# Kernel tuning notes

Measured on AMD Instinct MI355X. Metric: run time of the kernel, lower is better.

The kernel has to match this reference:

```python
import jax, jax.numpy as jnp
from jax import lax
import numpy as np

B, N, K = 8, 4096, 64          # clouds, points per cloud, max neighbors
N1, N2 = N // 2, N // 8        # fps ratio 0.5, then 0.25
R1, R2 = 0.2, 0.4              # ball-query radii


def setup_inputs() -> dict:
    key = jax.random.key(0)
    ks = jax.random.split(key, 7)
    def w(k, i, o):
        return jax.random.normal(k, (i, o), jnp.float32) / np.sqrt(i).astype(np.float32)
    return {
        "pos": jax.random.uniform(ks[0], (B, N, 3), jnp.float32),
        "w1a": w(ks[1], 3, 64),    "b1a": jnp.zeros(64, jnp.float32),
        "w1b": w(ks[2], 64, 64),   "b1b": jnp.zeros(64, jnp.float32),
        "w2a": w(ks[3], 67, 128),  "b2a": jnp.zeros(128, jnp.float32),
        "w2b": w(ks[4], 128, 128), "b2b": jnp.zeros(128, jnp.float32),
        "w3a": w(ks[5], 131, 256), "b3a": jnp.zeros(256, jnp.float32),
        "w3b": w(ks[6], 256, 1024),"b3b": jnp.zeros(1024, jnp.float32),
    }


def fps(pos, n_samples):
    # farthest point sampling, deterministic start at index 0. pos: [n, 3]
    d0 = jnp.sum((pos - pos[0]) ** 2, axis=-1)
    def step(mind, _):
        nxt = jnp.argmax(mind)
        d = jnp.sum((pos - pos[nxt]) ** 2, axis=-1)
        return jnp.minimum(mind, d), nxt
    _, idxs = lax.scan(step, d0, None, length=n_samples - 1)
    return jnp.concatenate([jnp.zeros((1,), idxs.dtype), idxs])


def ball_query(centers, pts, r):
    # up to K neighbors within radius r (nearest-first); centers are a subset of pts
    d2 = jnp.sum((centers[:, None, :] - pts[None, :, :]) ** 2, axis=-1)  # [M, n]
    neg = jnp.where(d2 <= r * r, -d2, -jnp.inf)
    vals, nbr = lax.top_k(neg, K)
    return nbr, vals > -jnp.inf  # [M, K] indices, validity mask


def mlp(x, w1, b1, w2, b2, relu_last):
    h = jax.nn.relu(x @ w1 + b1) @ w2 + b2
    return jax.nn.relu(h) if relu_last else h


def masked_max(h, mask):
    # max over neighbor axis; every center has itself as a valid neighbor
    return jnp.max(jnp.where(mask[..., None], h, -jnp.inf), axis=1)


def reference(pos, w1a, b1a, w1b, b1b, w2a, b2a, w2b, b2b, w3a, b3a, w3b, b3b):
    def single(p):  # p: [N, 3]
        # SA1: x is None -> per-edge input is relative position only
        idx1 = fps(p, N1)
        c1 = p[idx1]                                   # [N1, 3]
        nbr1, m1 = ball_query(c1, p, R1)               # [N1, K]
        rel1 = p[nbr1] - c1[:, None, :]                # [N1, K, 3]
        x1 = masked_max(mlp(rel1, w1a, b1a, w1b, b1b, True), m1)   # [N1, 64]
        # SA2: per-edge input is [x_j, pos_j - pos_i]
        idx2 = fps(c1, N2)
        c2 = c1[idx2]                                  # [N2, 3]
        nbr2, m2 = ball_query(c2, c1, R2)              # [N2, K]
        feat2 = jnp.concatenate([x1[nbr2], c1[nbr2] - c2[:, None, :]], axis=-1)  # [N2,K,67]
        x2 = masked_max(mlp(feat2, w2a, b2a, w2b, b2b, True), m2)  # [N2, 128]
        # Global SA: MLP on [x, pos] then global max pool
        g = mlp(jnp.concatenate([x2, c2], axis=-1), w3a, b3a, w3b, b3b, False)   # [N2,1024]
        return jnp.max(g, axis=0)                      # [1024]
    return jax.vmap(single)(pos)                       # [B, 1024]
```

## Files before the change

### kernel.cpp

```cpp
#include <hip/hip_runtime.h>
#include <cstdint>
#include <cstddef>


static constexpr int Bc = 8;
static constexpr int Np = 4096;
static constexpr int Kn = 64;
static constexpr int M1 = 2048;
static constexpr int M2 = 512;
static constexpr int LDX = 132;

#define DEVINL __device__ __forceinline__

DEVINL float d2_exact(float ax, float ay, float az, float bx, float by, float bz) {
    float dx = __fsub_rn(ax, bx);
    float dy = __fsub_rn(ay, by);
    float dz = __fsub_rn(az, bz);
    float xx = __fmul_rn(dx, dx);
    float yy = __fmul_rn(dy, dy);
    float zz = __fmul_rn(dz, dz);
    return __fadd_rn(__fadd_rn(xx, yy), zz);
}

template <int CTRL, int RM, int BM>
DEVINL unsigned long long dpp_max_step(unsigned long long k) {
    unsigned lo = (unsigned)k, hi = (unsigned)(k >> 32);
    unsigned slo = (unsigned)__builtin_amdgcn_update_dpp(0, (int)lo, CTRL, RM, BM, true);
    unsigned shi = (unsigned)__builtin_amdgcn_update_dpp(0, (int)hi, CTRL, RM, BM, true);
    unsigned long long s = ((unsigned long long)shi << 32) | (unsigned long long)slo;
    return s > k ? s : k;
}

DEVINL unsigned long long wave_max_u64_dpp(unsigned long long k) {
    k = dpp_max_step<0x111, 0xf, 0xf>(k);
    k = dpp_max_step<0x112, 0xf, 0xf>(k);
    k = dpp_max_step<0x114, 0xf, 0xf>(k);
    k = dpp_max_step<0x118, 0xf, 0xf>(k);
    k = dpp_max_step<0x142, 0xa, 0xf>(k);
    k = dpp_max_step<0x143, 0xc, 0xf>(k);
    return k;
}

DEVINL unsigned mort3(unsigned v) {
    return (v & 1u) | ((v & 2u) << 2) | ((v & 4u) << 4);
}

DEVINL unsigned cell_of(float x, float y, float z) {
    int ix = (int)(x * 8.0f); ix = ix < 0 ? 0 : (ix > 7 ? 7 : ix);
    int iy = (int)(y * 8.0f); iy = iy < 0 ? 0 : (iy > 7 ? 7 : iy);
    int iz = (int)(z * 8.0f); iz = iz < 0 ? 0 : (iz > 7 ? 7 : iz);
    return mort3((unsigned)ix) | (mort3((unsigned)iy) << 1) | (mort3((unsigned)iz) << 2);
}

DEVINL unsigned* scan512(unsigned* h0, unsigned* h1, int t) {
    unsigned* src = h0; unsigned* dst = h1;
    for (int d = 1; d < 512; d <<= 1) {
        unsigned v = src[t];
        if (t >= d) v += src[t - d];
        dst[t] = v;
        __syncthreads();
        unsigned* tmp = src; src = dst; dst = tmp;
    }
    return src;
}

__global__ __launch_bounds__(512)
void fps2x_kernel(const float* __restrict__ pos, float* __restrict__ c1,
                  float* __restrict__ c2, float* __restrict__ X) {
    constexpr int NT = 512;
    __shared__ float scx[Np], scy[Np], scz[Np];
    __shared__ unsigned spk[Np];
    __shared__ alignas(16) float s2c[M1 * 3];
    __shared__ alignas(16) float s3c[M2 * 3];
    __shared__ unsigned h0[512], h1[512];
    __shared__ unsigned long long slots[3];
    const int b = blockIdx.x;
    const int t = threadIdx.x;
    const int lane = t & 63;

    {
        constexpr int PT = Np / NT;
        const float* base = pos + (size_t)b * Np * 3;
        float gx[PT], gy[PT], gz[PT];
        unsigned gc[PT];
        #pragma unroll
        for (int j = 0; j < PT; ++j) {
            int p = j * NT + t;
            gx[j] = base[p * 3 + 0];
            gy[j] = base[p * 3 + 1];
            gz[j] = base[p * 3 + 2];
            gc[j] = cell_of(gx[j], gy[j], gz[j]);
        }
        float x0 = base[0], y0 = base[1], z0 = base[2];
        h0[t] = 0;
        if (t == 0) { slots[0] = 0; slots[1] = 0; slots[2] = 0; }
        __syncthreads();
        #pragma unroll
        for (int j = 0; j < PT; ++j) atomicAdd(&h0[gc[j]], 1u);
        __syncthreads();
        unsigned cnt = h0[t];
        unsigned* inc = scan512(h0, h1, t);
        inc[t] -= cnt;
        __syncthreads();
        #pragma unroll
        for (int j = 0; j < PT; ++j) {
            unsigned p = atomicAdd(&inc[gc[j]], 1u);
            scx[p] = gx[j]; scy[p] = gy[j]; scz[p] = gz[j];
            spk[p] = ((0xFFFu - (unsigned)(j * NT + t)) << 12) | p;
        }
        __syncthreads();

        float px[PT], py[PT], pz[PT], mind[PT];
        unsigned oi[PT];
        #pragma unroll
        for (int j = 0; j < PT; ++j) {
            int p = t * PT + j;
            px[j] = scx[p]; py[j] = scy[p]; pz[j] = scz[p];
            oi[j] = spk[p];
        }
        float lox = px[0], hix = px[0], loy = py[0], hiy = py[0], loz = pz[0], hiz = pz[0];
        #pragma unroll
        for (int j = 1; j < PT; ++j) {
            lox = fminf(lox, px[j]); hix = fmaxf(hix, px[j]);
            loy = fminf(loy, py[j]); hiy = fmaxf(hiy, py[j]);
            loz = fminf(loz, pz[j]); hiz = fmaxf(hiz, pz[j]);
        }

        unsigned long long ck = 0;
        #pragma unroll
        for (int j = 0; j < PT; ++j) {
            float d = d2_exact(px[j], py[j], pz[j], x0, y0, z0);
            mind[j] = d;
            unsigned long long kj =
                ((unsigned long long)__float_as_uint(d) << 24) | (unsigned long long)oi[j];
            if (kj > ck) ck = kj;
        }
        float bmax = __uint_as_float((unsigned)(ck >> 24));
        unsigned long long wkey = wave_max_u64_dpp(ck);
        if (lane == 63) atomicMax(&slots[1], wkey);
        if (t == 0) { s2c[0] = x0; s2c[1] = y0; s2c[2] = z0; }
        int rd = 1, wr = 2, rs = 0;
        for (int s = 1; s < M1; ++s) {
            __syncthreads();
            unsigned long long km = slots[rd];
            if (t == 0) slots[rs] = 0;
            unsigned spos = (unsigned)km & 0xFFFu;
            float cx = scx[spos], cy = scy[spos], cz = scz[spos];
            if (t == 0) {
                s2c[s * 3 + 0] = cx; s2c[s * 3 + 1] = cy; s2c[s * 3 + 2] = cz;
            }
            float dxv = fmaxf(fmaxf(lox - cx, cx - hix), 0.0f);
            float dyv = fmaxf(fmaxf(loy - cy, cy - hiy), 0.0f);
            float dzv = fmaxf(fmaxf(loz - cz, cz - hiz), 0.0f);
            float L = dxv * dxv + dyv * dyv + dzv * dzv;
            bool fire = (L * 0.999f <= bmax);
            if (fire) {
                unsigned long long nck = 0;
                #pragma unroll
                for (int j = 0; j < PT; ++j) {
                    float d = d2_exact(px[j], py[j], pz[j], cx, cy, cz);
                    float m = fminf(mind[j], d);
                    mind[j] = m;
                    unsigned long long kj =
                        ((unsigned long long)__float_as_uint(m) << 24) | (unsigned long long)oi[j];
                    if (kj > nck) nck = kj;
                }
                ck = nck;
                bmax = __uint_as_float((unsigned)(ck >> 24));
            }
            if (__ballot(fire) != 0ull) wkey = wave_max_u64_dpp(ck);
            if (lane == 63) atomicMax(&slots[wr], wkey);
            int nrd = wr; wr = rs; rs = rd; rd = nrd;
        }
    }
    __syncthreads();

    {
        const float4* s2c4 = (const float4*)s2c;
        float4* c1b = (float4*)(c1 + (size_t)b * M1 * 3);
        for (int i = t; i < M1 * 3 / 4; i += NT) c1b[i] = s2c4[i];
    }
    if (t == 0) { slots[0] = 0; slots[1] = 0; slots[2] = 0; }
    __syncthreads();

    {
        constexpr int PT = M1 / NT;
        float gx[PT], gy[PT], gz[PT];
        unsigned gc[PT];
        #pragma unroll
        for (int j = 0; j < PT; ++j) {
            int p = j * NT + t;
            gx[j] = s2c[p * 3 + 0];
            gy[j] = s2c[p * 3 + 1];
            gz[j] = s2c[p * 3 + 2];
            gc[j] = cell_of(gx[j], gy[j], gz[j]);
        }
        float x0 = s2c[0], y0 = s2c[1], z0 = s2c[2];
        h0[t] = 0;
        __syncthreads();
        #pragma unroll
        for (int j = 0; j < PT; ++j) atomicAdd(&h0[gc[j]], 1u);
        __syncthreads();
        unsigned cnt = h0[t];
        unsigned* inc = scan512(h0, h1, t);
        inc[t] -= cnt;
        __syncthreads();
        #pragma unroll
        for (int j = 0; j < PT; ++j) {
            unsigned p = atomicAdd(&inc[gc[j]], 1u);
            scx[p] = gx[j]; scy[p] = gy[j]; scz[p] = gz[j];
            spk[p] = ((0xFFFu - (unsigned)(j * NT + t)) << 12) | p;
        }
        __syncthreads();

        float px[PT], py[PT], pz[PT], mind[PT];
        unsigned oi[PT];
        #pragma unroll
        for (int j = 0; j < PT; ++j) {
            int p = t * PT + j;
            px[j] = scx[p]; py[j] = scy[p]; pz[j] = scz[p];
            oi[j] = spk[p];
        }
        float lox = px[0], hix = px[0], loy = py[0], hiy = py[0], loz = pz[0], hiz = pz[0];
        #pragma unroll
        for (int j = 1; j < PT; ++j) {
            lox = fminf(lox, px[j]); hix = fmaxf(hix, px[j]);
            loy = fminf(loy, py[j]); hiy = fmaxf(hiy, py[j]);
            loz = fminf(loz, pz[j]); hiz = fmaxf(hiz, pz[j]);
        }

        unsigned long long ck = 0;
        #pragma unroll
        for (int j = 0; j < PT; ++j) {
            float d = d2_exact(px[j], py[j], pz[j], x0, y0, z0);
            mind[j] = d;
            unsigned long long kj =
                ((unsigned long long)__float_as_uint(d) << 24) | (unsigned long long)oi[j];
            if (kj > ck) ck = kj;
        }
        float bmax = __uint_as_float((unsigned)(ck >> 24));
        unsigned long long wkey = wave_max_u64_dpp(ck);
        if (lane == 63) atomicMax(&slots[1], wkey);
        if (t == 0) { s3c[0] = x0; s3c[1] = y0; s3c[2] = z0; }
        int rd = 1, wr = 2, rs = 0;
        for (int s = 1; s < M2; ++s) {
            __syncthreads();
            unsigned long long km = slots[rd];
            if (t == 0) slots[rs] = 0;
            unsigned spos = (unsigned)km & 0xFFFu;
            float cx = scx[spos], cy = scy[spos], cz = scz[spos];
            if (t == 0) {
                s3c[s * 3 + 0] = cx; s3c[s * 3 + 1] = cy; s3c[s * 3 + 2] = cz;
            }
            float dxv = fmaxf(fmaxf(lox - cx, cx - hix), 0.0f);
            float dyv = fmaxf(fmaxf(loy - cy, cy - hiy), 0.0f);
            float dzv = fmaxf(fmaxf(loz - cz, cz - hiz), 0.0f);
            float L = dxv * dxv + dyv * dyv + dzv * dzv;
            bool fire = (L * 0.999f <= bmax);
            if (fire) {
                unsigned long long nck = 0;
                #pragma unroll
                for (int j = 0; j < PT; ++j) {
                    float d = d2_exact(px[j], py[j], pz[j], cx, cy, cz);
                    float m = fminf(mind[j], d);
                    mind[j] = m;
                    unsigned long long kj =
                        ((unsigned long long)__float_as_uint(m) << 24) | (unsigned long long)oi[j];
                    if (kj > nck) nck = kj;
                }
                ck = nck;
                bmax = __uint_as_float((unsigned)(ck >> 24));
            }
            if (__ballot(fire) != 0ull) wkey = wave_max_u64_dpp(ck);
            if (lane == 63) atomicMax(&slots[wr], wkey);
            int nrd = wr; wr = rs; rs = rd; rd = nrd;
        }
    }
    __syncthreads();

    {
        const float4* s3c4 = (const float4*)s3c;
        float4* c2b = (float4*)(c2 + (size_t)b * M2 * 3);
        for (int i = t; i < M2 * 3 / 4; i += NT) c2b[i] = s3c4[i];
        for (int s = t; s < M2; s += NT) {
            float* xr = X + (size_t)(b * M2 + s) * LDX;
            xr[128] = s3c[s * 3 + 0];
            xr[129] = s3c[s * 3 + 1];
            xr[130] = s3c[s * 3 + 2];
        }
    }
}

template <int NPT>
__global__ __launch_bounds__(256)
void bq_kernel(const float* __restrict__ pts, const float* __restrict__ ctr,
               int mshift, float r2, int* __restrict__ nbr) {
    constexpr int CH = NPT / 64;
    constexpr int CAP = 1024;
    __shared__ uint2 cbuf[4][CAP];
    const int lane = threadIdx.x & 63;
    const int wl = threadIdx.x >> 6;
    int w = __builtin_amdgcn_readfirstlane((int)(blockIdx.x * 4 + wl));
    const int b = w >> mshift;
    const float* pb = pts + (size_t)b * NPT * 3;
    const float* cp = ctr + (size_t)w * 3;
    float cx = cp[0], cy = cp[1], cz = cp[2];
    const unsigned r2b = __float_as_uint(r2);

    unsigned ub[CH];
    int cnt = 0;
    #pragma unroll
    for (int j = 0; j < CH; ++j) {
        int p = j * 64 + lane;
        float d = d2_exact(pb[p * 3 + 0], pb[p * 3 + 1], pb[p * 3 + 2], cx, cy, cz);
        ub[j] = __float_as_uint(d);
        cnt += __popcll(__ballot(ub[j] <= r2b));
    }
    int* out = nbr + (size_t)w * Kn;
    const unsigned long long lml = (1ull << lane) - 1ull;

    if (cnt <= Kn) {
        int basep = 0;
        #pragma unroll
        for (int j = 0; j < CH; ++j) {
            bool v = ub[j] <= r2b;
            unsigned long long mk = __ballot(v);
            if (v) out[basep + __popcll(mk & lml)] = j * 64 + lane;
            basep += __popcll(mk);
        }
        if (lane >= cnt) out[lane] = -1;
    } else if (cnt <= CAP) {
        uint2* buf = cbuf[wl];
        int basep = 0;
        #pragma unroll
        for (int j = 0; j < CH; ++j) {
            bool v = ub[j] <= r2b;
            unsigned long long mk = __ballot(v);
            if (v) buf[basep + __popcll(mk & lml)] =
                       make_uint2(ub[j], (unsigned)(j * 64 + lane));
            basep += __popcll(mk);
        }
        const int C2 = (cnt + 63) >> 6;
        unsigned cb[CAP / 64], ci[CAP / 64];
        #pragma unroll
        for (int e = 0; e < CAP / 64; ++e) {
            if (e >= C2) break;
            int p = e * 64 + lane;
            uint2 v = buf[p];
            cb[e] = (p < cnt) ? v.x : 0xFFFFFFFFu;
            ci[e] = v.y;
        }
        unsigned lo = 0, hi = r2b;
        while (lo < hi) {
            unsigned mid = lo + ((hi - lo) >> 1);
            int c = 0;
            #pragma unroll
            for (int e = 0; e < CAP / 64; ++e) {
                if (e >= C2) break;
                c += __popcll(__ballot(cb[e] <= mid));
            }
            if (c >= Kn) hi = mid; else lo = mid + 1;
        }
        const unsigned tt = lo;
        int cntLess = 0;
        #pragma unroll
        for (int e = 0; e < CAP / 64; ++e) {
            if (e >= C2) break;
            cntLess += __popcll(__ballot(cb[e] < tt));
        }
        const int quota = Kn - cntLess;
        int baseLt = 0, eqseen = 0;
        #pragma unroll
        for (int e = 0; e < CAP / 64; ++e) {
            if (e >= C2) break;
            bool lt = cb[e] < tt;
            bool eq = cb[e] == tt;
            unsigned long long mlt = __ballot(lt);
            unsigned long long meq = __ballot(eq);
            if (lt) out[baseLt + __popcll(mlt & lml)] = (int)ci[e];
            if (eq) {
                int rr = eqseen + __popcll(meq & lml);
                if (rr < quota) out[cntLess + rr] = (int)ci[e];
            }
            baseLt += __popcll(mlt);
            eqseen += __popcll(meq);
        }
    } else {
        unsigned lo = 0, hi = r2b;
        while (lo < hi) {
            unsigned mid = lo + ((hi - lo) >> 1);
            int c = 0;
            #pragma unroll
            for (int j = 0; j < CH; ++j) c += __popcll(__ballot(ub[j] <= mid));
            if (c >= Kn) hi = mid; else lo = mid + 1;
        }
        const unsigned tt = lo;
        int cntLess = 0;
        #pragma unroll
        for (int j = 0; j < CH; ++j) cntLess += __popcll(__ballot(ub[j] < tt));
        const int quota = Kn - cntLess;
        int baseLt = 0, eqseen = 0;
        #pragma unroll
        for (int j = 0; j < CH; ++j) {
            bool lt = ub[j] < tt;
            bool eq = ub[j] == tt;
            unsigned long long mlt = __ballot(lt);
            unsigned long long meq = __ballot(eq);
            if (lt) out[baseLt + __popcll(mlt & lml)] = j * 64 + lane;
            if (eq) {
                int rr = eqseen + __popcll(meq & lml);
                if (rr < quota) out[cntLess + rr] = j * 64 + lane;
            }
            baseLt += __popcll(mlt);
            eqseen += __popcll(meq);
        }
    }
}

__global__ __launch_bounds__(256)
void mlp1_kernel(const float* __restrict__ pos, const float* __restrict__ c1,
                 const int* __restrict__ nbr, const float* __restrict__ w1aT,
                 const float* __restrict__ w1bT, const float* __restrict__ b1b,
                 float* __restrict__ x1) {
    const int lane = threadIdx.x & 63;
    int w = __builtin_amdgcn_readfirstlane((int)(blockIdx.x * 4 + (threadIdx.x >> 6)));
    const int b = w >> 11;
    const int ii = nbr[(size_t)w * Kn + lane];
    const bool valid = ii >= 0;
    const int i2 = valid ? ii : 0;
    const float* pp = pos + ((size_t)b * Np + i2) * 3;
    const float* cc = c1 + (size_t)w * 3;
    float rx = pp[0] - cc[0], ry = pp[1] - cc[1], rz = pp[2] - cc[2];
    float h1[64];
    #pragma unroll
    for (int h = 0; h < 64; ++h) {
        float4 wv = ((const float4*)w1aT)[h];
        float a = fmaf(rx, wv.x, fmaf(ry, wv.y, fmaf(rz, wv.z, wv.w)));
        h1[h] = fmaxf(a, 0.0f);
    }
    float* orow = x1 + (size_t)w * 64;
    for (int c4 = 0; c4 < 16; ++c4) {
        float v4[4];
        #pragma unroll
        for (int cq = 0; cq < 4; ++cq) {
            int c = c4 * 4 + cq;
            float acc = b1b[c];
            const float4* wr = (const float4*)(w1bT + (size_t)c * 64);
            #pragma unroll
            for (int q = 0; q < 16; ++q) {
                float4 wv = wr[q];
                acc = fmaf(h1[4 * q + 0], wv.x, acc);
                acc = fmaf(h1[4 * q + 1], wv.y, acc);
                acc = fmaf(h1[4 * q + 2], wv.z, acc);
                acc = fmaf(h1[4 * q + 3], wv.w, acc);
            }
            float v = fmaxf(acc, 0.0f);
            v = valid ? v : -__builtin_inff();
            #pragma unroll
            for (int o = 32; o > 0; o >>= 1) v = fmaxf(v, __shfl_xor(v, o, 64));
            v4[cq] = v;
        }
        if (lane == 0)
            ((float4*)orow)[c4] = make_float4(v4[0], v4[1], v4[2], v4[3]);
    }
}

__global__ __launch_bounds__(256)
void mlp2_kernel(const float* __restrict__ x1, const float* __restrict__ c1,
                 const float* __restrict__ c2, const int* __restrict__ nbr2,
                 const float* __restrict__ w2aT, const float* __restrict__ w2bT,
                 const float* __restrict__ b2b, float* __restrict__ X) {
    const int lane = threadIdx.x & 63;
    int w = __builtin_amdgcn_readfirstlane((int)(blockIdx.x * 4 + (threadIdx.x >> 6)));
    const int b = w >> 9;
    const int ii = nbr2[(size_t)w * Kn + lane];
    const bool valid = ii >= 0;
    const int i2 = valid ? ii : 0;

    float x[68];
    const float4* xr = (const float4*)(x1 + ((size_t)b * M1 + i2) * 64);
    #pragma unroll
    for (int q = 0; q < 16; ++q) {
        float4 v = xr[q];
        x[4 * q + 0] = v.x; x[4 * q + 1] = v.y;
        x[4 * q + 2] = v.z; x[4 * q + 3] = v.w;
    }
    const float* cc = c2 + (size_t)w * 3;
    const float* cp = c1 + ((size_t)b * M1 + i2) * 3;
    x[64] = cp[0] - cc[0];
    x[65] = cp[1] - cc[1];
    x[66] = cp[2] - cc[2];
    x[67] = 0.0f;

    float h1[128];
    #pragma unroll
    for (int h = 0; h < 128; ++h) {
        const float4* r4 = (const float4*)(w2aT + (size_t)h * 80);
        float acc = 0.0f;
        #pragma unroll
        for (int q = 0; q < 16; ++q) {
            float4 wv = r4[q];
            acc = fmaf(x[4 * q + 0], wv.x, acc);
            acc = fmaf(x[4 * q + 1], wv.y, acc);
            acc = fmaf(x[4 * q + 2], wv.z, acc);
            acc = fmaf(x[4 * q + 3], wv.w, acc);
        }
        float4 tl = r4[16];
        acc = fmaf(x[64], tl.x, acc);
        acc = fmaf(x[65], tl.y, acc);
        acc = fmaf(x[66], tl.z, acc);
        acc += tl.w;
        h1[h] = fmaxf(acc, 0.0f);
    }
    float* orow = X + (size_t)w * LDX;
    for (int c4 = 0; c4 < 32; ++c4) {
        float v4[4];
        #pragma unroll
        for (int cq = 0; cq < 4; ++cq) {
            int c = c4 * 4 + cq;
            float acc = b2b[c];
            const float4* wr = (const float4*)(w2bT + (size_t)c * 128);
            #pragma unroll
            for (int q = 0; q < 32; ++q) {
                float4 wv = wr[q];
                acc = fmaf(h1[4 * q + 0], wv.x, acc);
                acc = fmaf(h1[4 * q + 1], wv.y, acc);
                acc = fmaf(h1[4 * q + 2], wv.z, acc);
                acc = fmaf(h1[4 * q + 3], wv.w, acc);
            }
            float v = fmaxf(acc, 0.0f);
            v = valid ? v : -__builtin_inff();
            #pragma unroll
            for (int o = 32; o > 0; o >>= 1) v = fmaxf(v, __shfl_xor(v, o, 64));
            v4[cq] = v;
        }
        if (lane == 0) {
            orow[c4 * 4 + 0] = v4[0]; orow[c4 * 4 + 1] = v4[1];
            orow[c4 * 4 + 2] = v4[2]; orow[c4 * 4 + 3] = v4[3];
        }
    }
}

__global__ __launch_bounds__(256)
void gemm1_kernel(const float* __restrict__ X, const float* __restrict__ w3a,
                  const float* __restrict__ b3a, float* __restrict__ H) {
    const int r = blockIdx.x;
    const int c = threadIdx.x;
    const float* xr = X + (size_t)r * LDX;
    float acc = b3a[c];
    for (int i = 0; i < 131; ++i)
        acc = fmaf(xr[i], w3a[(size_t)i * 256 + c], acc);
    H[(size_t)r * 256 + c] = fmaxf(acc, 0.0f);
}

__global__ __launch_bounds__(256)
void gemm2_kernel(const float* __restrict__ H, const float* __restrict__ w3b,
                  float* __restrict__ part) {
    __shared__ float As[32][33];
    __shared__ float Bs[32][64];
    __shared__ float red[8][64];
    const int bidx = blockIdx.x;
    const int nt = bidx & 15;
    const int mt = (bidx >> 4) & 15;
    const int b = bidx >> 8;
    const int row0 = b * M2 + mt * 32;
    const int col0 = nt * 64;
    const int t = threadIdx.x;
    const int rg = t >> 5, cg = t & 31;

    float acc[4][2] = {{0.f, 0.f}, {0.f, 0.f}, {0.f, 0.f}, {0.f, 0.f}};
    for (int k0 = 0; k0 < 256; k0 += 32) {
        #pragma unroll
        for (int q = 0; q < 4; ++q) {
            int id = t + q * 256;
            As[id >> 5][id & 31] = H[(size_t)(row0 + (id >> 5)) * 256 + k0 + (id & 31)];
        }
        #pragma unroll
        for (int q = 0; q < 8; ++q) {
            int id = t + q * 256;
            Bs[id >> 6][id & 63] = w3b[(size_t)(k0 + (id >> 6)) * 1024 + col0 + (id & 63)];
        }
        __syncthreads();
        #pragma unroll
        for (int kk = 0; kk < 32; ++kk) {
            float b0 = Bs[kk][cg * 2 + 0];
            float b1 = Bs[kk][cg * 2 + 1];
            #pragma unroll
            for (int j = 0; j < 4; ++j) {
                float a = As[rg * 4 + j][kk];
                acc[j][0] = fmaf(a, b0, acc[j][0]);
                acc[j][1] = fmaf(a, b1, acc[j][1]);
            }
        }
        __syncthreads();
    }
    float m0 = fmaxf(fmaxf(acc[0][0], acc[1][0]), fmaxf(acc[2][0], acc[3][0]));
    float m1 = fmaxf(fmaxf(acc[0][1], acc[1][1]), fmaxf(acc[2][1], acc[3][1]));
    red[rg][cg * 2 + 0] = m0;
    red[rg][cg * 2 + 1] = m1;
    __syncthreads();
    if (t < 64) {
        float v = red[0][t];
        #pragma unroll
        for (int q = 1; q < 8; ++q) v = fmaxf(v, red[q][t]);
        part[((size_t)b * 16 + mt) * 1024 + col0 + t] = v;
    }
}

__global__ __launch_bounds__(256)
void rmax_kernel(const float* __restrict__ part, const float* __restrict__ b3b,
                 float* __restrict__ out) {
    int i = blockIdx.x * 256 + threadIdx.x;
    int b = i >> 10, c = i & 1023;
    float v = -__builtin_inff();
    #pragma unroll
    for (int tt = 0; tt < 16; ++tt)
        v = fmaxf(v, part[((size_t)b * 16 + tt) * 1024 + c]);
    out[i] = v + b3b[c];
}

__global__ __launch_bounds__(256)
void prep_kernel(const float* __restrict__ w1a, const float* __restrict__ b1a,
                 const float* __restrict__ w1b, const float* __restrict__ w2a,
                 const float* __restrict__ b2a, const float* __restrict__ w2b,
                 float* __restrict__ w1aT, float* __restrict__ w1bT,
                 float* __restrict__ w2aT, float* __restrict__ w2bT) {
    int i = blockIdx.x * 256 + threadIdx.x;
    if (i < 64 * 4) {
        int h = i >> 2, d = i & 3;
        w1aT[i] = (d < 3) ? w1a[d * 64 + h] : b1a[h];
    }
    if (i < 64 * 64) {
        int c = i >> 6, h = i & 63;
        w1bT[i] = w1b[h * 64 + c];
    }
    if (i < 128 * 80) {
        int h = i / 80, d = i - h * 80;
        w2aT[i] = (d < 67) ? w2a[d * 128 + h] : ((d == 67) ? b2a[h] : 0.0f);
    }
    {
        int c = i >> 7, h = i & 127;
        w2bT[i] = w2b[h * 128 + c];
    }
}

extern "C" void kernel_launch(void* const* d_in, const int* in_sizes, int n_in,
                              void* d_out, int out_size, void* d_ws, size_t ws_size,
                              hipStream_t stream) {
    const float* pos = (const float*)d_in[0];
    const float* w1a = (const float*)d_in[1];
    const float* b1a = (const float*)d_in[2];
    const float* w1b = (const float*)d_in[3];
    const float* b1b = (const float*)d_in[4];
    const float* w2a = (const float*)d_in[5];
    const float* b2a = (const float*)d_in[6];
    const float* w2b = (const float*)d_in[7];
    const float* b2b = (const float*)d_in[8];
    const float* w3a = (const float*)d_in[9];
    const float* b3a = (const float*)d_in[10];
    const float* w3b = (const float*)d_in[11];
    const float* b3b = (const float*)d_in[12];
    float* out = (float*)d_out;

    char* ws = (char*)d_ws;
    size_t off = 0;
    auto alloc = [&](size_t bytes) -> char* {
        char* p = ws + off;
        off += (bytes + 255) & ~(size_t)255;
        return p;
    };
    float* c1   = (float*)alloc(sizeof(float) * Bc * M1 * 3);
    float* c2   = (float*)alloc(sizeof(float) * Bc * M2 * 3);
    int*   nbr1 = (int*)alloc(sizeof(int) * Bc * M1 * Kn);
    int*   nbr2 = (int*)alloc(sizeof(int) * Bc * M2 * Kn);
    float* x1   = (float*)alloc(sizeof(float) * Bc * M1 * 64);
    float* X    = (float*)alloc(sizeof(float) * Bc * M2 * LDX);
    float* H    = (float*)alloc(sizeof(float) * Bc * M2 * 256);
    float* part = (float*)alloc(sizeof(float) * Bc * 16 * 1024);
    float* w1aT = (float*)alloc(sizeof(float) * 64 * 4);
    float* w1bT = (float*)alloc(sizeof(float) * 64 * 64);
    float* w2aT = (float*)alloc(sizeof(float) * 128 * 80);
    float* w2bT = (float*)alloc(sizeof(float) * 128 * 128);

    prep_kernel<<<dim3(64), dim3(256), 0, stream>>>(w1a, b1a, w1b, w2a, b2a, w2b,
                                                    w1aT, w1bT, w2aT, w2bT);
    fps2x_kernel<<<dim3(Bc), dim3(512), 0, stream>>>(pos, c1, c2, X);
    bq_kernel<Np><<<dim3(Bc * M1 / 4), dim3(256), 0, stream>>>(
        pos, c1, 11, (float)(0.2 * 0.2), nbr1);
    mlp1_kernel<<<dim3(Bc * M1 / 4), dim3(256), 0, stream>>>(
        pos, c1, nbr1, w1aT, w1bT, b1b, x1);
    bq_kernel<M1><<<dim3(Bc * M2 / 4), dim3(256), 0, stream>>>(
        c1, c2, 9, (float)(0.4 * 0.4), nbr2);
    mlp2_kernel<<<dim3(Bc * M2 / 4), dim3(256), 0, stream>>>(
        x1, c1, c2, nbr2, w2aT, w2bT, b2b, X);
    gemm1_kernel<<<dim3(Bc * M2), dim3(256), 0, stream>>>(X, w3a, b3a, H);
    gemm2_kernel<<<dim3(Bc * 16 * 16), dim3(256), 0, stream>>>(H, w3b, part);
    rmax_kernel<<<dim3(32), dim3(256), 0, stream>>>(part, b3b, out);
}
```

Measured before the change: 2.557 ms.

## Fuse pipeline stages into four kernels, keeping neighbor lists in shared memory

Merges weight prep into the FPS kernel, ball query 1 with MLP1, ball query 2 with MLP2 and the first global GEMM, and the final row-max into the second GEMM using a last-block atomic counter. Neighbor indices and per-center features now stay in shared memory instead of global buffers, and five launches are removed. The cost is higher register and shared-memory pressure in the fused kernels, plus a counter that must be reset by the earlier kernel. The SA2 ball query also drops the mid-size candidate-buffer path and always uses binary search when there are more than K neighbors.

```diff
diff --git a/kernel.cpp b/kernel.cpp
--- a/kernel.cpp
+++ b/kernel.cpp
@@ -8,7 +8,6 @@
 static constexpr int Kn = 64;
 static constexpr int M1 = 2048;
 static constexpr int M2 = 512;
-static constexpr int LDX = 132;
 
 #define DEVINL __device__ __forceinline__
 
@@ -66,7 +65,12 @@
 
 __global__ __launch_bounds__(512)
 void fps2x_kernel(const float* __restrict__ pos, float* __restrict__ c1,
-                  float* __restrict__ c2, float* __restrict__ X) {
+                  float* __restrict__ c2,
+                  const float* __restrict__ w1a, const float* __restrict__ b1a,
+                  const float* __restrict__ w1b, const float* __restrict__ w2a,
+                  const float* __restrict__ b2a, const float* __restrict__ w2b,
+                  float* __restrict__ w1aT, float* __restrict__ w1bT,
+                  float* __restrict__ w2aT, float* __restrict__ w2bT) {
     constexpr int NT = 512;
     __shared__ float scx[Np], scy[Np], scz[Np];
     __shared__ unsigned spk[Np];
@@ -77,6 +81,25 @@
     const int b = blockIdx.x;
     const int t = threadIdx.x;
     const int lane = t & 63;
+
+    for (int i = b * NT + t; i < 128 * 128; i += Bc * NT) {
+        if (i < 64 * 4) {
+            int h = i >> 2, d = i & 3;
+            w1aT[i] = (d < 3) ? w1a[d * 64 + h] : b1a[h];
+        }
+        if (i < 64 * 64) {
+            int c = i >> 6, h = i & 63;
+            w1bT[i] = w1b[h * 64 + c];
+        }
+        if (i < 128 * 80) {
+            int h = i / 80, d = i - h * 80;
+            w2aT[i] = (d < 67) ? w2a[d * 128 + h] : ((d == 67) ? b2a[h] : 0.0f);
+        }
+        {
+            int c = i >> 7, h = i & 127;
+            w2bT[i] = w2b[h * 128 + c];
+        }
+    }
 
     {
         constexpr int PT = Np / NT;
@@ -282,30 +305,26 @@
         const float4* s3c4 = (const float4*)s3c;
         float4* c2b = (float4*)(c2 + (size_t)b * M2 * 3);
         for (int i = t; i < M2 * 3 / 4; i += NT) c2b[i] = s3c4[i];
-        for (int s = t; s < M2; s += NT) {
-            float* xr = X + (size_t)(b * M2 + s) * LDX;
-            xr[128] = s3c[s * 3 + 0];
-            xr[129] = s3c[s * 3 + 1];
-            xr[130] = s3c[s * 3 + 2];
-        }
-    }
-}
-
-template <int NPT>
+    }
+}
+
 __global__ __launch_bounds__(256)
-void bq_kernel(const float* __restrict__ pts, const float* __restrict__ ctr,
-               int mshift, float r2, int* __restrict__ nbr) {
+void bqmlp1_kernel(const float* __restrict__ pos, const float* __restrict__ c1,
+                   const float* __restrict__ w1aT, const float* __restrict__ w1bT,
+                   const float* __restrict__ b1b, float* __restrict__ x1) {
+    constexpr int NPT = Np;
     constexpr int CH = NPT / 64;
     constexpr int CAP = 1024;
     __shared__ uint2 cbuf[4][CAP];
+    __shared__ int nout[4][Kn];
     const int lane = threadIdx.x & 63;
     const int wl = threadIdx.x >> 6;
     int w = __builtin_amdgcn_readfirstlane((int)(blockIdx.x * 4 + wl));
-    const int b = w >> mshift;
-    const float* pb = pts + (size_t)b * NPT * 3;
-    const float* cp = ctr + (size_t)w * 3;
+    const int b = w >> 11;
+    const float* pb = pos + (size_t)b * NPT * 3;
+    const float* cp = c1 + (size_t)w * 3;
     float cx = cp[0], cy = cp[1], cz = cp[2];
-    const unsigned r2b = __float_as_uint(r2);
+    const unsigned r2b = __float_as_uint(0.04f);
 
     unsigned ub[CH];
     int cnt = 0;
@@ -316,7 +335,7 @@
         ub[j] = __float_as_uint(d);
         cnt += __popcll(__ballot(ub[j] <= r2b));
     }
-    int* out = nbr + (size_t)w * Kn;
+    int* out = &nout[wl][0];
     const unsigned long long lml = (1ull << lane) - 1ull;
 
     if (cnt <= Kn) {
@@ -415,22 +434,13 @@
             eqseen += __popcll(meq);
         }
     }
-}
-
-__global__ __launch_bounds__(256)
-void mlp1_kernel(const float* __restrict__ pos, const float* __restrict__ c1,
-                 const int* __restrict__ nbr, const float* __restrict__ w1aT,
-                 const float* __restrict__ w1bT, const float* __restrict__ b1b,
-                 float* __restrict__ x1) {
-    const int lane = threadIdx.x & 63;
-    int w = __builtin_amdgcn_readfirstlane((int)(blockIdx.x * 4 + (threadIdx.x >> 6)));
-    const int b = w >> 11;
-    const int ii = nbr[(size_t)w * Kn + lane];
+    __syncthreads();
+
+    const int ii = nout[wl][lane];
     const bool valid = ii >= 0;
     const int i2 = valid ? ii : 0;
     const float* pp = pos + ((size_t)b * Np + i2) * 3;
-    const float* cc = c1 + (size_t)w * 3;
-    float rx = pp[0] - cc[0], ry = pp[1] - cc[1], rz = pp[2] - cc[2];
+    float rx = pp[0] - cx, ry = pp[1] - cy, rz = pp[2] - cz;
     float h1[64];
     #pragma unroll
     for (int h = 0; h < 64; ++h) {
@@ -466,99 +476,177 @@
 }
 
 __global__ __launch_bounds__(256)
-void mlp2_kernel(const float* __restrict__ x1, const float* __restrict__ c1,
-                 const float* __restrict__ c2, const int* __restrict__ nbr2,
-                 const float* __restrict__ w2aT, const float* __restrict__ w2bT,
-                 const float* __restrict__ b2b, float* __restrict__ X) {
+void bqmlp2g1_kernel(const float* __restrict__ c1, const float* __restrict__ c2,
+                     const float* __restrict__ x1, const float* __restrict__ w2aT,
+                     const float* __restrict__ w2bT, const float* __restrict__ b2b,
+                     const float* __restrict__ w3a, const float* __restrict__ b3a,
+                     float* __restrict__ H, unsigned* __restrict__ counter) {
+    constexpr int NPT = M1;
+    constexpr int CH = NPT / 64;
+    __shared__ int nout[4][Kn];
+    __shared__ float sX[4][132];
     const int lane = threadIdx.x & 63;
-    int w = __builtin_amdgcn_readfirstlane((int)(blockIdx.x * 4 + (threadIdx.x >> 6)));
+    const int wl = threadIdx.x >> 6;
+    int w = __builtin_amdgcn_readfirstlane((int)(blockIdx.x * 4 + wl));
     const int b = w >> 9;
-    const int ii = nbr2[(size_t)w * Kn + lane];
-    const bool valid = ii >= 0;
-    const int i2 = valid ? ii : 0;
-
-    float x[68];
-    const float4* xr = (const float4*)(x1 + ((size_t)b * M1 + i2) * 64);
+    if (blockIdx.x == 0 && threadIdx.x == 0) *counter = 0;
+    const float* pb = c1 + (size_t)b * NPT * 3;
+    const float* cp = c2 + (size_t)w * 3;
+    float cx = cp[0], cy = cp[1], cz = cp[2];
+    const unsigned r2b = __float_as_uint(0.16000001f);
+
+    unsigned ub[CH];
+    int cnt = 0;
     #pragma unroll
-    for (int q = 0; q < 16; ++q) {
-        float4 v = xr[q];
-        x[4 * q + 0] = v.x; x[4 * q + 1] = v.y;
-        x[4 * q + 2] = v.z; x[4 * q + 3] = v.w;
-    }
-    const float* cc = c2 + (size_t)w * 3;
-    const float* cp = c1 + ((size_t)b * M1 + i2) * 3;
-    x[64] = cp[0] - cc[0];
-    x[65] = cp[1] - cc[1];
-    x[66] = cp[2] - cc[2];
-    x[67] = 0.0f;
-
-    float h1[128];
-    #pragma unroll
-    for (int h = 0; h < 128; ++h) {
-        const float4* r4 = (const float4*)(w2aT + (size_t)h * 80);
-        float acc = 0.0f;
+    for (int j = 0; j < CH; ++j) {
+        int p = j * 64 + lane;
+        float d = d2_exact(pb[p * 3 + 0], pb[p * 3 + 1], pb[p * 3 + 2], cx, cy, cz);
+        ub[j] = __float_as_uint(d);
+        cnt += __popcll(__ballot(ub[j] <= r2b));
+    }
+    int* out = &nout[wl][0];
+    const unsigned long long lml = (1ull << lane) - 1ull;
+
+    if (cnt <= Kn) {
+        int basep = 0;
+        #pragma unroll
+        for (int j = 0; j < CH; ++j) {
+            bool v = ub[j] <= r2b;
+            unsigned long long mk = __ballot(v);
+            if (v) out[basep + __popcll(mk & lml)] = j * 64 + lane;
+            basep += __popcll(mk);
+        }
+        if (lane >= cnt) out[lane] = -1;
+    } else {
+        unsigned lo = 0, hi = r2b;
+        while (lo < hi) {
+            unsigned mid = lo + ((hi - lo) >> 1);
+            int c = 0;
+            #pragma unroll
+            for (int j = 0; j < CH; ++j) c += __popcll(__ballot(ub[j] <= mid));
+            if (c >= Kn) hi = mid; else lo = mid + 1;
+        }
+        const unsigned tt = lo;
+        int cntLess = 0;
+        #pragma unroll
+        for (int j = 0; j < CH; ++j) cntLess += __popcll(__ballot(ub[j] < tt));
+        const int quota = Kn - cntLess;
+        int baseLt = 0, eqseen = 0;
+        #pragma unroll
+        for (int j = 0; j < CH; ++j) {
+            bool lt = ub[j] < tt;
+            bool eq = ub[j] == tt;
+            unsigned long long mlt = __ballot(lt);
+            unsigned long long meq = __ballot(eq);
+            if (lt) out[baseLt + __popcll(mlt & lml)] = j * 64 + lane;
+            if (eq) {
+                int rr = eqseen + __popcll(meq & lml);
+                if (rr < quota) out[cntLess + rr] = j * 64 + lane;
+            }
+            baseLt += __popcll(mlt);
+            eqseen += __popcll(meq);
+        }
+    }
+    __syncthreads();
+
+    {
+        const int ii = nout[wl][lane];
+        const bool valid = ii >= 0;
+        const int i2 = valid ? ii : 0;
+        float x[68];
+        const float4* xr = (const float4*)(x1 + ((size_t)b * M1 + i2) * 64);
         #pragma unroll
         for (int q = 0; q < 16; ++q) {
-            float4 wv = r4[q];
-            acc = fmaf(x[4 * q + 0], wv.x, acc);
-            acc = fmaf(x[4 * q + 1], wv.y, acc);
-            acc = fmaf(x[4 * q + 2], wv.z, acc);
-            acc = fmaf(x[4 * q + 3], wv.w, acc);
-        }
-        float4 tl = r4[16];
-        acc = fmaf(x[64], tl.x, acc);
-        acc = fmaf(x[65], tl.y, acc);
-        acc = fmaf(x[66], tl.z, acc);
-        acc += tl.w;
-        h1[h] = fmaxf(acc, 0.0f);
-    }
-    float* orow = X + (size_t)w * LDX;
-    for (int c4 = 0; c4 < 32; ++c4) {
-        float v4[4];
-        #pragma unroll
-        for (int cq = 0; cq < 4; ++cq) {
-            int c = c4 * 4 + cq;
-            float acc = b2b[c];
-            const float4* wr = (const float4*)(w2bT + (size_t)c * 128);
-            #pragma unroll
-            for (int q = 0; q < 32; ++q) {
-                float4 wv = wr[q];
-                acc = fmaf(h1[4 * q + 0], wv.x, acc);
-                acc = fmaf(h1[4 * q + 1], wv.y, acc);
-                acc = fmaf(h1[4 * q + 2], wv.z, acc);
-                acc = fmaf(h1[4 * q + 3], wv.w, acc);
-            }
-            float v = fmaxf(acc, 0.0f);
-            v = valid ? v : -__builtin_inff();
-            #pragma unroll
-            for (int o = 32; o > 0; o >>= 1) v = fmaxf(v, __shfl_xor(v, o, 64));
-            v4[cq] = v;
+            float4 v = xr[q];
+            x[4 * q + 0] = v.x; x[4 * q + 1] = v.y;
+            x[4 * q + 2] = v.z; x[4 * q + 3] = v.w;
+        }
+        const float* cpn = c1 + ((size_t)b * M1 + i2) * 3;
+        x[64] = cpn[0] - cx;
+        x[65] = cpn[1] - cy;
+        x[66] = cpn[2] - cz;
+        x[67] = 0.0f;
+
+        float h1[128];
+        #pragma unroll
+        for (int h = 0; h < 128; ++h) {
+            const float4* r4 = (const float4*)(w2aT + (size_t)h * 80);
+            float acc = 0.0f;
+            #pragma unroll
+            for (int q = 0; q < 16; ++q) {
+                float4 wv = r4[q];
+                acc = fmaf(x[4 * q + 0], wv.x, acc);
+                acc = fmaf(x[4 * q + 1], wv.y, acc);
+                acc = fmaf(x[4 * q + 2], wv.z, acc);
+                acc = fmaf(x[4 * q + 3], wv.w, acc);
+            }
+            float4 tl = r4[16];
+            acc = fmaf(x[64], tl.x, acc);
+            acc = fmaf(x[65], tl.y, acc);
+            acc = fmaf(x[66], tl.z, acc);
+            acc += tl.w;
+            h1[h] = fmaxf(acc, 0.0f);
+        }
+        for (int c4 = 0; c4 < 32; ++c4) {
+            float v4[4];
+            #pragma unroll
+            for (int cq = 0; cq < 4; ++cq) {
+                int c = c4 * 4 + cq;
+                float acc = b2b[c];
+                const float4* wr = (const float4*)(w2bT + (size_t)c * 128);
+                #pragma unroll
+                for (int q = 0; q < 32; ++q) {
+                    float4 wv = wr[q];
+                    acc = fmaf(h1[4 * q + 0], wv.x, acc);
+                    acc = fmaf(h1[4 * q + 1], wv.y, acc);
+                    acc = fmaf(h1[4 * q + 2], wv.z, acc);
+                    acc = fmaf(h1[4 * q + 3], wv.w, acc);
+                }
+                float v = fmaxf(acc, 0.0f);
+                v = valid ? v : -__builtin_inff();
+                #pragma unroll
+                for (int o = 32; o > 0; o >>= 1) v = fmaxf(v, __shfl_xor(v, o, 64));
+                v4[cq] = v;
+            }
+            if (lane == 0) {
+                sX[wl][c4 * 4 + 0] = v4[0]; sX[wl][c4 * 4 + 1] = v4[1];
+                sX[wl][c4 * 4 + 2] = v4[2]; sX[wl][c4 * 4 + 3] = v4[3];
+            }
         }
         if (lane == 0) {
-            orow[c4 * 4 + 0] = v4[0]; orow[c4 * 4 + 1] = v4[1];
-            orow[c4 * 4 + 2] = v4[2]; orow[c4 * 4 + 3] = v4[3];
-        }
+            sX[wl][128] = cx; sX[wl][129] = cy; sX[wl][130] = cz;
+            sX[wl][131] = 0.0f;
+        }
+    }
+    __syncthreads();
+
+    {
+        const int t = threadIdx.x;
+        float bias = b3a[t];
+        float a0 = bias, a1 = bias, a2 = bias, a3 = bias;
+        for (int i = 0; i < 131; ++i) {
+            float wv = w3a[(size_t)i * 256 + t];
+            a0 = fmaf(sX[0][i], wv, a0);
+            a1 = fmaf(sX[1][i], wv, a1);
+            a2 = fmaf(sX[2][i], wv, a2);
+            a3 = fmaf(sX[3][i], wv, a3);
+        }
+        const size_t r0 = (size_t)blockIdx.x * 4;
+        H[(r0 + 0) * 256 + t] = fmaxf(a0, 0.0f);
+        H[(r0 + 1) * 256 + t] = fmaxf(a1, 0.0f);
+        H[(r0 + 2) * 256 + t] = fmaxf(a2, 0.0f);
+        H[(r0 + 3) * 256 + t] = fmaxf(a3, 0.0f);
     }
 }
 
 __global__ __launch_bounds__(256)
-void gemm1_kernel(const float* __restrict__ X, const float* __restrict__ w3a,
-                  const float* __restrict__ b3a, float* __restrict__ H) {
-    const int r = blockIdx.x;
-    const int c = threadIdx.x;
-    const float* xr = X + (size_t)r * LDX;
-    float acc = b3a[c];
-    for (int i = 0; i < 131; ++i)
-        acc = fmaf(xr[i], w3a[(size_t)i * 256 + c], acc);
-    H[(size_t)r * 256 + c] = fmaxf(acc, 0.0f);
-}
-
-__global__ __launch_bounds__(256)
-void gemm2_kernel(const float* __restrict__ H, const float* __restrict__ w3b,
-                  float* __restrict__ part) {
+void gemm2rmax_kernel(const float* __restrict__ H, const float* __restrict__ w3b,
+                      float* __restrict__ part, unsigned* __restrict__ counter,
+                      const float* __restrict__ b3b, float* __restrict__ out) {
     __shared__ float As[32][33];
     __shared__ float Bs[32][64];
     __shared__ float red[8][64];
+    __shared__ int islast;
     const int bidx = blockIdx.x;
     const int nt = bidx & 15;
     const int mt = (bidx >> 4) & 15;
@@ -605,42 +693,23 @@
         for (int q = 1; q < 8; ++q) v = fmaxf(v, red[q][t]);
         part[((size_t)b * 16 + mt) * 1024 + col0 + t] = v;
     }
-}
-
-__global__ __launch_bounds__(256)
-void rmax_kernel(const float* __restrict__ part, const float* __restrict__ b3b,
-                 float* __restrict__ out) {
-    int i = blockIdx.x * 256 + threadIdx.x;
-    int b = i >> 10, c = i & 1023;
-    float v = -__builtin_inff();
-    #pragma unroll
-    for (int tt = 0; tt < 16; ++tt)
-        v = fmaxf(v, part[((size_t)b * 16 + tt) * 1024 + c]);
-    out[i] = v + b3b[c];
-}
-
-__global__ __launch_bounds__(256)
-void prep_kernel(const float* __restrict__ w1a, const float* __restrict__ b1a,
-                 const float* __restrict__ w1b, const float* __restrict__ w2a,
-                 const float* __restrict__ b2a, const float* __restrict__ w2b,
-                 float* __restrict__ w1aT, float* __restrict__ w1bT,
-                 float* __restrict__ w2aT, float* __restrict__ w2bT) {
-    int i = blockIdx.x * 256 + threadIdx.x;
-    if (i < 64 * 4) {
-        int h = i >> 2, d = i & 3;
-        w1aT[i] = (d < 3) ? w1a[d * 64 + h] : b1a[h];
-    }
-    if (i < 64 * 64) {
-        int c = i >> 6, h = i & 63;
-        w1bT[i] = w1b[h * 64 + c];
-    }
-    if (i < 128 * 80) {
-        int h = i / 80, d = i - h * 80;
-        w2aT[i] = (d < 67) ? w2a[d * 128 + h] : ((d == 67) ? b2a[h] : 0.0f);
-    }
-    {
-        int c = i >> 7, h = i & 127;
-        w2bT[i] = w2b[h * 128 + c];
+    __threadfence();
+    __syncthreads();
+    if (t == 0) {
+        unsigned r = atomicAdd(counter, 1u);
+        islast = (r == (unsigned)(gridDim.x - 1)) ? 1 : 0;
+    }
+    __syncthreads();
+    if (islast) {
+        __threadfence();
+        for (int i = t; i < Bc * 1024; i += 256) {
+            int bb = i >> 10, c = i & 1023;
+            float v = -__builtin_inff();
+            #pragma unroll
+            for (int tt2 = 0; tt2 < 16; ++tt2)
+                v = fmaxf(v, part[((size_t)bb * 16 + tt2) * 1024 + c]);
+            out[i] = v + b3b[c];
+        }
     }
 }
 
@@ -671,29 +740,21 @@
     };
     float* c1   = (float*)alloc(sizeof(float) * Bc * M1 * 3);
     float* c2   = (float*)alloc(sizeof(float) * Bc * M2 * 3);
-    int*   nbr1 = (int*)alloc(sizeof(int) * Bc * M1 * Kn);
-    int*   nbr2 = (int*)alloc(sizeof(int) * Bc * M2 * Kn);
     float* x1   = (float*)alloc(sizeof(float) * Bc * M1 * 64);
-    float* X    = (float*)alloc(sizeof(float) * Bc * M2 * LDX);
     float* H    = (float*)alloc(sizeof(float) * Bc * M2 * 256);
     float* part = (float*)alloc(sizeof(float) * Bc * 16 * 1024);
     float* w1aT = (float*)alloc(sizeof(float) * 64 * 4);
     float* w1bT = (float*)alloc(sizeof(float) * 64 * 64);
     float* w2aT = (float*)alloc(sizeof(float) * 128 * 80);
     float* w2bT = (float*)alloc(sizeof(float) * 128 * 128);
-
-    prep_kernel<<<dim3(64), dim3(256), 0, stream>>>(w1a, b1a, w1b, w2a, b2a, w2b,
-                                                    w1aT, w1bT, w2aT, w2bT);
-    fps2x_kernel<<<dim3(Bc), dim3(512), 0, stream>>>(pos, c1, c2, X);
-    bq_kernel<Np><<<dim3(Bc * M1 / 4), dim3(256), 0, stream>>>(
-        pos, c1, 11, (float)(0.2 * 0.2), nbr1);
-    mlp1_kernel<<<dim3(Bc * M1 / 4), dim3(256), 0, stream>>>(
-        pos, c1, nbr1, w1aT, w1bT, b1b, x1);
-    bq_kernel<M1><<<dim3(Bc * M2 / 4), dim3(256), 0, stream>>>(
-        c1, c2, 9, (float)(0.4 * 0.4), nbr2);
-    mlp2_kernel<<<dim3(Bc * M2 / 4), dim3(256), 0, stream>>>(
-        x1, c1, c2, nbr2, w2aT, w2bT, b2b, X);
-    gemm1_kernel<<<dim3(Bc * M2), dim3(256), 0, stream>>>(X, w3a, b3a, H);
-    gemm2_kernel<<<dim3(Bc * 16 * 16), dim3(256), 0, stream>>>(H, w3b, part);
-    rmax_kernel<<<dim3(32), dim3(256), 0, stream>>>(part, b3b, out);
-}
+    unsigned* counter = (unsigned*)alloc(sizeof(unsigned) * 16);
+
+    fps2x_kernel<<<dim3(Bc), dim3(512), 0, stream>>>(
+        pos, c1, c2, w1a, b1a, w1b, w2a, b2a, w2b, w1aT, w1bT, w2aT, w2bT);
+    bqmlp1_kernel<<<dim3(Bc * M1 / 4), dim3(256), 0, stream>>>(
+        pos, c1, w1aT, w1bT, b1b, x1);
+    bqmlp2g1_kernel<<<dim3(Bc * M2 / 4), dim3(256), 0, stream>>>(
+        c1, c2, x1, w2aT, w2bT, b2b, w3a, b3a, H, counter);
+    gemm2rmax_kernel<<<dim3(Bc * 16 * 16), dim3(256), 0, stream>>>(
+        H, w3b, part, counter, b3b, out);
+}
```

New measurement: 2.868 ms. +12.2%, slower.

## Replace FPS atomic slot reduction with per-wave partials and halve block size

Applied to the files above, without the earlier changes.

The FPS kernel now runs with 256 threads (4 waves) instead of 512. Each wave writes its best key and the winning point's coordinates into a double-buffered shared array, and every thread picks the maximum of the four entries. This replaces the LDS atomicMax on rotating slots and the dependent coordinate lookup. The spatial grid drops to 256 cells in plain row-major order, with a smaller scan. Per-step synchronisation latency should fall, in exchange for each thread owning twice as many points.

```diff
diff --git a/kernel.cpp b/kernel.cpp
--- a/kernel.cpp
+++ b/kernel.cpp
@@ -41,20 +41,16 @@
     return k;
 }
 
-DEVINL unsigned mort3(unsigned v) {
-    return (v & 1u) | ((v & 2u) << 2) | ((v & 4u) << 4);
-}
-
 DEVINL unsigned cell_of(float x, float y, float z) {
-    int ix = (int)(x * 8.0f); ix = ix < 0 ? 0 : (ix > 7 ? 7 : ix);
+    int ix = (int)(x * 4.0f); ix = ix < 0 ? 0 : (ix > 3 ? 3 : ix);
     int iy = (int)(y * 8.0f); iy = iy < 0 ? 0 : (iy > 7 ? 7 : iy);
     int iz = (int)(z * 8.0f); iz = iz < 0 ? 0 : (iz > 7 ? 7 : iz);
-    return mort3((unsigned)ix) | (mort3((unsigned)iy) << 1) | (mort3((unsigned)iz) << 2);
-}
-
-DEVINL unsigned* scan512(unsigned* h0, unsigned* h1, int t) {
+    return ((unsigned)ix << 6) | ((unsigned)iy << 3) | (unsigned)iz;
+}
+
+DEVINL unsigned* scan256(unsigned* h0, unsigned* h1, int t) {
     unsigned* src = h0; unsigned* dst = h1;
-    for (int d = 1; d < 512; d <<= 1) {
+    for (int d = 1; d < 256; d <<= 1) {
         unsigned v = src[t];
         if (t >= d) v += src[t - d];
         dst[t] = v;
@@ -64,19 +60,35 @@
     return src;
 }
 
-__global__ __launch_bounds__(512)
+DEVINL void sel2(unsigned long long ka, float4 ca, unsigned long long kb, float4 cb,
+                 unsigned long long& ko, float4& co) {
+    bool tk = kb > ka;
+    ko = tk ? kb : ka;
+    co.x = tk ? cb.x : ca.x;
+    co.y = tk ? cb.y : ca.y;
+    co.z = tk ? cb.z : ca.z;
+}
+
+DEVINL unsigned long long readlane63_u64(unsigned long long v) {
+    unsigned lo = (unsigned)__builtin_amdgcn_readlane((int)(unsigned)v, 63);
+    unsigned hi = (unsigned)__builtin_amdgcn_readlane((int)(unsigned)(v >> 32), 63);
+    return ((unsigned long long)hi << 32) | (unsigned long long)lo;
+}
+
+__global__ __launch_bounds__(256)
 void fps2x_kernel(const float* __restrict__ pos, float* __restrict__ c1,
                   float* __restrict__ c2, float* __restrict__ X) {
-    constexpr int NT = 512;
+    constexpr int NT = 256;
     __shared__ float scx[Np], scy[Np], scz[Np];
     __shared__ unsigned spk[Np];
     __shared__ alignas(16) float s2c[M1 * 3];
     __shared__ alignas(16) float s3c[M2 * 3];
-    __shared__ unsigned h0[512], h1[512];
-    __shared__ unsigned long long slots[3];
+    __shared__ unsigned h0[256], h1[256];
+    __shared__ alignas(16) unsigned long long pK[2][4];
+    __shared__ alignas(16) float4 pC[2][4];
     const int b = blockIdx.x;
     const int t = threadIdx.x;
-    const int lane = t & 63;
+    const int wid = t >> 6;
 
     {
         constexpr int PT = Np / NT;
@@ -93,13 +105,12 @@
         }
         float x0 = base[0], y0 = base[1], z0 = base[2];
         h0[t] = 0;
-        if (t == 0) { slots[0] = 0; slots[1] = 0; slots[2] = 0; }
         __syncthreads();
         #pragma unroll
         for (int j = 0; j < PT; ++j) atomicAdd(&h0[gc[j]], 1u);
         __syncthreads();
         unsigned cnt = h0[t];
-        unsigned* inc = scan512(h0, h1, t);
+        unsigned* inc = scan256(h0, h1, t);
         inc[t] -= cnt;
         __syncthreads();
         #pragma unroll
@@ -127,25 +138,32 @@
         }
 
         unsigned long long ck = 0;
+        float bx = 0.f, by = 0.f, bz = 0.f;
         #pragma unroll
         for (int j = 0; j < PT; ++j) {
             float d = d2_exact(px[j], py[j], pz[j], x0, y0, z0);
             mind[j] = d;
             unsigned long long kj =
                 ((unsigned long long)__float_as_uint(d) << 24) | (unsigned long long)oi[j];
-            if (kj > ck) ck = kj;
+            if (kj > ck) { ck = kj; bx = px[j]; by = py[j]; bz = pz[j]; }
         }
         float bmax = __uint_as_float((unsigned)(ck >> 24));
-        unsigned long long wkey = wave_max_u64_dpp(ck);
-        if (lane == 63) atomicMax(&slots[1], wkey);
+        unsigned long long wred = wave_max_u64_dpp(ck);
+        unsigned long long wk = readlane63_u64(wred);
+        if (ck == wk) { pK[1][wid] = ck; pC[1][wid] = make_float4(bx, by, bz, 0.f); }
         if (t == 0) { s2c[0] = x0; s2c[1] = y0; s2c[2] = z0; }
-        int rd = 1, wr = 2, rs = 0;
         for (int s = 1; s < M1; ++s) {
             __syncthreads();
-            unsigned long long km = slots[rd];
-            if (t == 0) slots[rs] = 0;
-            unsigned spos = (unsigned)km & 0xFFFu;
-            float cx = scx[spos], cy = scy[spos], cz = scz[spos];
+            const int rb = s & 1;
+            const ulonglong2* pk2 = (const ulonglong2*)pK[rb];
+            ulonglong2 k01 = pk2[0], k23 = pk2[1];
+            float4 q0 = pC[rb][0], q1 = pC[rb][1], q2 = pC[rb][2], q3 = pC[rb][3];
+            unsigned long long m01, m23, mw;
+            float4 s01, s23, sw;
+            sel2(k01.x, q0, k01.y, q1, m01, s01);
+            sel2(k23.x, q2, k23.y, q3, m23, s23);
+            sel2(m01, s01, m23, s23, mw, sw);
+            float cx = sw.x, cy = sw.y, cz = sw.z;
             if (t == 0) {
                 s2c[s * 3 + 0] = cx; s2c[s * 3 + 1] = cy; s2c[s * 3 + 2] = cz;
             }
@@ -156,6 +174,7 @@
             bool fire = (L * 0.999f <= bmax);
             if (fire) {
                 unsigned long long nck = 0;
+                float nbx = 0.f, nby = 0.f, nbz = 0.f;
                 #pragma unroll
                 for (int j = 0; j < PT; ++j) {
                     float d = d2_exact(px[j], py[j], pz[j], cx, cy, cz);
@@ -163,14 +182,17 @@
                     mind[j] = m;
                     unsigned long long kj =
                         ((unsigned long long)__float_as_uint(m) << 24) | (unsigned long long)oi[j];
-                    if (kj > nck) nck = kj;
+                    if (kj > nck) { nck = kj; nbx = px[j]; nby = py[j]; nbz = pz[j]; }
                 }
-                ck = nck;
+                ck = nck; bx = nbx; by = nby; bz = nbz;
                 bmax = __uint_as_float((unsigned)(ck >> 24));
             }
-            if (__ballot(fire) != 0ull) wkey = wave_max_u64_dpp(ck);
-            if (lane == 63) atomicMax(&slots[wr], wkey);
-            int nrd = wr; wr = rs; rs = rd; rd = nrd;
+            if (__ballot(fire) != 0ull) {
+                wred = wave_max_u64_dpp(ck);
+                wk = readlane63_u64(wred);
+            }
+            const int nb = (s + 1) & 1;
+            if (ck == wk) { pK[nb][wid] = ck; pC[nb][wid] = make_float4(bx, by, bz, 0.f); }
         }
     }
     __syncthreads();
@@ -180,7 +202,6 @@
         float4* c1b = (float4*)(c1 + (size_t)b * M1 * 3);
         for (int i = t; i < M1 * 3 / 4; i += NT) c1b[i] = s2c4[i];
     }
-    if (t == 0) { slots[0] = 0; slots[1] = 0; slots[2] = 0; }
     __syncthreads();
 
     {
@@ -202,7 +223,7 @@
         for (int j = 0; j < PT; ++j) atomicAdd(&h0[gc[j]], 1u);
         __syncthreads();
         unsigned cnt = h0[t];
-        unsigned* inc = scan512(h0, h1, t);
+        unsigned* inc = scan256(h0, h1, t);
         inc[t] -= cnt;
         __syncthreads();
         #pragma unroll
@@ -230,25 +251,32 @@
         }
 
         unsigned long long ck = 0;
+        float bx = 0.f, by = 0.f, bz = 0.f;
         #pragma unroll
         for (int j = 0; j < PT; ++j) {
             float d = d2_exact(px[j], py[j], pz[j], x0, y0, z0);
             mind[j] = d;
             unsigned long long kj =
                 ((unsigned long long)__float_as_uint(d) << 24) | (unsigned long long)oi[j];
-            if (kj > ck) ck = kj;
+            if (kj > ck) { ck = kj; bx = px[j]; by = py[j]; bz = pz[j]; }
         }
         float bmax = __uint_as_float((unsigned)(ck >> 24));
-        unsigned long long wkey = wave_max_u64_dpp(ck);
-        if (lane == 63) atomicMax(&slots[1], wkey);
+        unsigned long long wred = wave_max_u64_dpp(ck);
+        unsigned long long wk = readlane63_u64(wred);
+        if (ck == wk) { pK[1][wid] = ck; pC[1][wid] = make_float4(bx, by, bz, 0.f); }
         if (t == 0) { s3c[0] = x0; s3c[1] = y0; s3c[2] = z0; }
-        int rd = 1, wr = 2, rs = 0;
         for (int s = 1; s < M2; ++s) {
             __syncthreads();
-            unsigned long long km = slots[rd];
-            if (t == 0) slots[rs] = 0;
-            unsigned spos = (unsigned)km & 0xFFFu;
-            float cx = scx[spos], cy = scy[spos], cz = scz[spos];
+            const int rb = s & 1;
+            const ulonglong2* pk2 = (const ulonglong2*)pK[rb];
+            ulonglong2 k01 = pk2[0], k23 = pk2[1];
+            float4 q0 = pC[rb][0], q1 = pC[rb][1], q2 = pC[rb][2], q3 = pC[rb][3];
+            unsigned long long m01, m23, mw;
+            float4 s01, s23, sw;
+            sel2(k01.x, q0, k01.y, q1, m01, s01);
+            sel2(k23.x, q2, k23.y, q3, m23, s23);
+            sel2(m01, s01, m23, s23, mw, sw);
+            float cx = sw.x, cy = sw.y, cz = sw.z;
             if (t == 0) {
                 s3c[s * 3 + 0] = cx; s3c[s * 3 + 1] = cy; s3c[s * 3 + 2] = cz;
             }
@@ -259,6 +287,7 @@
             bool fire = (L * 0.999f <= bmax);
             if (fire) {
                 unsigned long long nck = 0;
+                float nbx = 0.f, nby = 0.f, nbz = 0.f;
                 #pragma unroll
                 for (int j = 0; j < PT; ++j) {
                     float d = d2_exact(px[j], py[j], pz[j], cx, cy, cz);
@@ -266,14 +295,17 @@
                     mind[j] = m;
                     unsigned long long kj =
                         ((unsigned long long)__float_as_uint(m) << 24) | (unsigned long long)oi[j];
-                    if (kj > nck) nck = kj;
+                    if (kj > nck) { nck = kj; nbx = px[j]; nby = py[j]; nbz = pz[j]; }
                 }
-                ck = nck;
+                ck = nck; bx = nbx; by = nby; bz = nbz;
                 bmax = __uint_as_float((unsigned)(ck >> 24));
             }
-            if (__ballot(fire) != 0ull) wkey = wave_max_u64_dpp(ck);
-            if (lane == 63) atomicMax(&slots[wr], wkey);
-            int nrd = wr; wr = rs; rs = rd; rd = nrd;
+            if (__ballot(fire) != 0ull) {
+                wred = wave_max_u64_dpp(ck);
+                wk = readlane63_u64(wred);
+            }
+            const int nb = (s + 1) & 1;
+            if (ck == wk) { pK[nb][wid] = ck; pC[nb][wid] = make_float4(bx, by, bz, 0.f); }
         }
     }
     __syncthreads();
@@ -684,7 +716,7 @@
 
     prep_kernel<<<dim3(64), dim3(256), 0, stream>>>(w1a, b1a, w1b, w2a, b2a, w2b,
                                                     w1aT, w1bT, w2aT, w2bT);
-    fps2x_kernel<<<dim3(Bc), dim3(512), 0, stream>>>(pos, c1, c2, X);
+    fps2x_kernel<<<dim3(Bc), dim3(256), 0, stream>>>(pos, c1, c2, X);
     bq_kernel<Np><<<dim3(Bc * M1 / 4), dim3(256), 0, stream>>>(
         pos, c1, 11, (float)(0.2 * 0.2), nbr1);
     mlp1_kernel<<<dim3(Bc * M1 / 4), dim3(256), 0, stream>>>(
```

Result: slower. 4.027 ms (+57.5%).
